# Performance work log

Measured on AMD Instinct MI355X. Metric: run time of the kernel, lower is better.

Reference implementation:

```python
import jax, jax.numpy as jnp
import numpy as np

N = 100000
E = 1600000
H = 128
M = 256
L = 6
G = 512          # number of graphs in the batch
A = 95           # num_atom_types
EXTRA = 3        # input_dim - 1
EPS = 1e-5


def swish(x):
    return x * jax.nn.sigmoid(x)


def setup_inputs() -> dict:
    key = jax.random.key(0)
    ks = jax.random.split(key, 16)
    z = jax.random.randint(ks[0], (N, 1), 0, A).astype(jnp.float32)
    extra = jax.random.normal(ks[1], (N, EXTRA), dtype=jnp.float32)
    x = jnp.concatenate([z, extra], axis=1)                     # [N, 4]
    edge_index = jax.random.randint(ks[2], (2, E), 0, N)        # [2, E]
    batch = jnp.sort(jax.random.randint(ks[3], (N,), 0, G))     # [N]
    s = 0.02
    z_embed = jax.random.normal(ks[4], (A, H), dtype=jnp.float32) * s
    extra_w = jax.random.normal(ks[5], (H, EXTRA), dtype=jnp.float32) * (1.0 / np.sqrt(EXTRA))
    extra_b = jnp.zeros((H,), jnp.float32)
    conv_w = jax.random.normal(ks[6], (L, H, H), dtype=jnp.float32) * (1.0 / np.sqrt(H))
    conv_b = jnp.zeros((L, H), jnp.float32)
    gamma = jnp.ones((L, H), jnp.float32)
    beta = jnp.zeros((L, H), jnp.float32)
    mean_scale = jnp.ones((L, H), jnp.float32)
    mlp_w1 = jax.random.normal(ks[7], (L, M, H), dtype=jnp.float32) * (1.0 / np.sqrt(H))
    mlp_b1 = jnp.zeros((L, M), jnp.float32)
    mlp_w2 = jax.random.normal(ks[8], (L, H, M), dtype=jnp.float32) * (1.0 / np.sqrt(M))
    mlp_b2 = jnp.zeros((L, H), jnp.float32)
    return dict(x=x, edge_index=edge_index, batch=batch, z_embed=z_embed,
                extra_w=extra_w, extra_b=extra_b, conv_w=conv_w, conv_b=conv_b,
                gamma=gamma, beta=beta, mean_scale=mean_scale,
                mlp_w1=mlp_w1, mlp_b1=mlp_b1, mlp_w2=mlp_w2, mlp_b2=mlp_b2)


def gnn_forward(x, edge_index, batch, z_embed, extra_w, extra_b, conv_w, conv_b,
                gamma, beta, mean_scale, mlp_w1, mlp_b1, mlp_w2, mlp_b2):
    z = x[:, 0].astype(jnp.int32)
    h = z_embed[z] + x[:, 1:] @ extra_w.T + extra_b                 # [N, H]

    # GCN: add self loops, symmetric normalization (computed once; graph is static)
    loop = jnp.arange(N)
    src = jnp.concatenate([edge_index[0], loop])
    dst = jnp.concatenate([edge_index[1], loop])
    deg = jax.ops.segment_sum(jnp.ones_like(dst, jnp.float32), dst, num_segments=N)
    dinv = jnp.where(deg > 0, jax.lax.rsqrt(jnp.maximum(deg, 1.0)), 0.0)
    norm = (dinv[src] * dinv[dst])[:, None]                         # [E+N, 1]

    cnt = jax.ops.segment_sum(jnp.ones((N,), jnp.float32), batch, num_segments=G)[:, None]
    cnt = jnp.maximum(cnt, 1.0)

    for i in range(L):
        h_res = h
        # GCNConv
        xw = h @ conv_w[i].T
        agg = jax.ops.segment_sum(xw[src] * norm, dst, num_segments=N) + conv_b[i]
        # GraphNorm: gamma * (x - alpha*mean) / sqrt(var + eps) + beta, per graph
        mean = jax.ops.segment_sum(agg, batch, num_segments=G) / cnt   # [G, H]
        sub = agg - mean_scale[i] * mean[batch]
        var = jax.ops.segment_sum(sub * sub, batch, num_segments=G) / cnt
        hn = gamma[i] * sub * jax.lax.rsqrt(var[batch] + EPS) + beta[i]
        ha = swish(hn)
        # residual MLP
        h = swish(swish(ha @ mlp_w1[i].T + mlp_b1[i]) @ mlp_w2[i].T + mlp_b2[i]) + h_res
    return h


def reference(x, edge_index, batch, z_embed, extra_w, extra_b, conv_w, conv_b,
              gamma, beta, mean_scale, mlp_w1, mlp_b1, mlp_w2, mlp_b2):
    return gnn_forward(x, edge_index, batch, z_embed, extra_w, extra_b, conv_w, conv_b,
                       gamma, beta, mean_scale, mlp_w1, mlp_b1, mlp_w2, mlp_b2)
```

## Files before the change

### kernel.cpp

```cpp
#include <hip/hip_runtime.h>

#define NN 100000
#define EE 1600000
#define HH 128
#define MM 256
#define LL 6
#define GG 512
#define SCAN_NB ((NN + 1023) / 1024)

typedef __attribute__((ext_vector_type(8))) short short8;
typedef __attribute__((ext_vector_type(4))) float floatx4;

__device__ __forceinline__ float swishf(float v) {
    return v / (1.0f + __expf(-v));
}

__device__ __forceinline__ unsigned short f2bf(float f) {
    unsigned u = __builtin_bit_cast(unsigned, f);
    unsigned r = u + 0x7FFFu + ((u >> 16) & 1u);
    return (unsigned short)(r >> 16);
}

__device__ __forceinline__ float bf2f(unsigned short u) {
    return __builtin_bit_cast(float, (unsigned)u << 16);
}

__device__ __forceinline__ float2 bf2f2(unsigned u) {
    float2 r;
    r.x = __builtin_bit_cast(float, u << 16);
    r.y = __builtin_bit_cast(float, u & 0xFFFF0000u);
    return r;
}

__device__ __forceinline__ unsigned cvt2bf(float a, float b) {
    unsigned r;
    asm("v_cvt_pk_bf16_f32 %0, %1, %2" : "=v"(r) : "v"(a), "v"(b));
    return r;
}

__device__ __forceinline__ void unpack8(uint4 v, float* a) {
    float2 p0 = bf2f2(v.x), p1 = bf2f2(v.y), p2 = bf2f2(v.z), p3 = bf2f2(v.w);
    a[0] = p0.x; a[1] = p0.y; a[2] = p1.x; a[3] = p1.y;
    a[4] = p2.x; a[5] = p2.y; a[6] = p3.x; a[7] = p3.y;
}

__device__ __forceinline__ uint4 pack8(const float* o) {
    uint4 pk;
    pk.x = cvt2bf(o[0], o[1]);
    pk.y = cvt2bf(o[2], o[3]);
    pk.z = cvt2bf(o[4], o[5]);
    pk.w = cvt2bf(o[6], o[7]);
    return pk;
}

__device__ __forceinline__ uint2 pack4(const float* o) {
    uint2 pk;
    pk.x = cvt2bf(o[0], o[1]);
    pk.y = cvt2bf(o[2], o[3]);
    return pk;
}

__global__ void k_embed(const float* __restrict__ x, const float* __restrict__ z_embed,
                        const float* __restrict__ ew, const float* __restrict__ eb,
                        unsigned short* __restrict__ hb) {
    int idx = blockIdx.x * blockDim.x + threadIdx.x;
    if (idx >= NN * 32) return;
    int n = idx >> 5;
    int c0 = (idx & 31) << 2;
    const float* xr = x + (size_t)n * 4;
    int z = (int)xr[0];
    float x1 = xr[1], x2 = xr[2], x3 = xr[3];
    const float* ze = z_embed + (size_t)z * HH + c0;
    float o[4];
#pragma unroll
    for (int j = 0; j < 4; ++j) {
        int c = c0 + j;
        o[j] = ze[j] + x1 * ew[c * 3 + 0] + x2 * ew[c * 3 + 1] + x3 * ew[c * 3 + 2] + eb[c];
    }
    *(uint2*)(hb + (size_t)n * HH + c0) = pack4(o);
}

__global__ void k_f2bf3(const float* __restrict__ s1, unsigned short* __restrict__ d1, int n1,
                        const float* __restrict__ s2, unsigned short* __restrict__ d2, int n2,
                        const float* __restrict__ s3, unsigned short* __restrict__ d3, int n3) {
    int i = blockIdx.x * blockDim.x + threadIdx.x;
    if (i < n1) {
        d1[i] = f2bf(s1[i]);
    } else if (i < n1 + n2) {
        d2[i - n1] = f2bf(s2[i - n1]);
    } else if (i < n1 + n2 + n3) {
        d3[i - n1 - n2] = f2bf(s3[i - n1 - n2]);
    }
}

__global__ __launch_bounds__(256) void k_degree_p(const int* __restrict__ dst,
                                                  int* __restrict__ deg) {
    int part = blockIdx.x & 7;
    int blk = blockIdx.x >> 3;
    int nb = gridDim.x >> 3;
    int lo = (int)((long long)part * NN / 8);
    int hi = (int)((long long)(part + 1) * NN / 8);
    for (int e = blk * 256 + threadIdx.x; e < EE; e += nb * 256) {
        int d = dst[e];
        if (d >= lo && d < hi) atomicAdd(&deg[d], 1);
    }
}

__global__ void k_dinv(const int* __restrict__ deg, float* __restrict__ dinv) {
    int n = blockIdx.x * blockDim.x + threadIdx.x;
    if (n < NN) dinv[n] = rsqrtf((float)(deg[n] + 1));
}

__global__ void k_scan1(const int* __restrict__ deg, int* __restrict__ bsum) {
    __shared__ int sd[256];
    int t = threadIdx.x;
    int base = blockIdx.x * 1024 + t * 4;
    int s = 0;
#pragma unroll
    for (int j = 0; j < 4; ++j) {
        int i = base + j;
        if (i < NN) s += deg[i];
    }
    sd[t] = s;
    __syncthreads();
    for (int off = 128; off > 0; off >>= 1) {
        if (t < off) sd[t] += sd[t + off];
        __syncthreads();
    }
    if (t == 0) bsum[blockIdx.x] = sd[0];
}

__global__ void k_scan2(const int* __restrict__ bsum, int* __restrict__ boff) {
    __shared__ int sd[128];
    int t = threadIdx.x;
    int v = (t < SCAN_NB) ? bsum[t] : 0;
    sd[t] = v;
    __syncthreads();
    for (int off = 1; off < 128; off <<= 1) {
        int u = (t >= off) ? sd[t - off] : 0;
        __syncthreads();
        sd[t] += u;
        __syncthreads();
    }
    boff[t] = sd[t] - v;
}

__global__ void k_scan3(const int* __restrict__ deg, const int* __restrict__ boff,
                        int* __restrict__ rowptr) {
    __shared__ int sd[256];
    int t = threadIdx.x;
    int base = blockIdx.x * 1024 + t * 4;
    int v[4];
    int s = 0;
#pragma unroll
    for (int j = 0; j < 4; ++j) {
        int i = base + j;
        v[j] = (i < NN) ? deg[i] : 0;
        s += v[j];
    }
    sd[t] = s;
    __syncthreads();
    for (int off = 1; off < 256; off <<= 1) {
        int u = (t >= off) ? sd[t - off] : 0;
        __syncthreads();
        sd[t] += u;
        __syncthreads();
    }
    int run = boff[blockIdx.x] + sd[t] - s;
#pragma unroll
    for (int j = 0; j < 4; ++j) {
        int i = base + j;
        if (i < NN) rowptr[i] = run;
        if (i == NN - 1) rowptr[NN] = run + v[j];
        run += v[j];
    }
}

__global__ __launch_bounds__(256) void k_fill_p(const int* __restrict__ ei,
                                                const int* __restrict__ rowptr,
                                                int* __restrict__ cursor,
                                                int* __restrict__ col) {
    int part = blockIdx.x & 7;
    int blk = blockIdx.x >> 3;
    int nb = gridDim.x >> 3;
    int lo = (int)((long long)part * NN / 8);
    int hi = (int)((long long)(part + 1) * NN / 8);
    for (int e = blk * 256 + threadIdx.x; e < EE; e += nb * 256) {
        int d = ei[EE + e];
        if (d >= lo && d < hi) {
            int p = atomicAdd(&cursor[d], 1);
            col[rowptr[d] + p] = ei[e];
        }
    }
}

__global__ void k_gptr(const int* __restrict__ batch, int* __restrict__ gptr) {
    int n = blockIdx.x * blockDim.x + threadIdx.x;
    if (n >= NN) return;
    int b = batch[n];
    int pb = (n == 0) ? -1 : batch[n - 1];
    for (int g = pb + 1; g <= b; ++g) gptr[g] = n;
    if (n == NN - 1) {
        for (int g = b + 1; g <= GG; ++g) gptr[g] = NN;
    }
}

__global__ __launch_bounds__(256) void k_conv(const unsigned short* __restrict__ A,
                                              const unsigned short* __restrict__ B,
                                              const float* __restrict__ dinv,
                                              unsigned short* __restrict__ Cb) {
    __shared__ unsigned short Bs[128][HH + 8];
    const int tid = threadIdx.x;
    const int wave = tid >> 6;
    const int lane = tid & 63;
    const int quad = lane >> 4;
    const int l16 = lane & 15;
    const int wr = (wave & 1) << 6;
    const int wc = (wave >> 1) << 6;
    const int rowBase = blockIdx.x * 128;

    for (int i = tid; i < 128 * (HH / 8); i += 256) {
        int r = i / (HH / 8);
        int kk = (i % (HH / 8)) * 8;
        int rho = (r & 64) | ((r & 3) << 4) | ((r >> 2) & 15);
        *(uint4*)(&Bs[rho][kk]) = *(const uint4*)(B + (size_t)r * HH + kk);
    }

    floatx4 acc[4][4];
    const floatx4 zed = {0.f, 0.f, 0.f, 0.f};
#pragma unroll
    for (int i = 0; i < 4; ++i)
#pragma unroll
        for (int j = 0; j < 4; ++j) acc[i][j] = zed;

    int ar[4];
#pragma unroll
    for (int i = 0; i < 4; ++i) {
        int r = rowBase + wr + (i << 4) + l16;
        ar[i] = r < NN ? r : NN - 1;
    }

    __syncthreads();

#pragma unroll
    for (int ks = 0; ks < HH / 32; ++ks) {
        int k = (ks << 5) + (quad << 3);
        short8 a[4], b[4];
#pragma unroll
        for (int i = 0; i < 4; ++i) a[i] = *(const short8*)(A + (size_t)ar[i] * HH + k);
#pragma unroll
        for (int j = 0; j < 4; ++j) b[j] = *(const short8*)(&Bs[wc + (j << 4) + l16][k]);
#pragma unroll
        for (int i = 0; i < 4; ++i)
#pragma unroll
            for (int j = 0; j < 4; ++j)
                acc[i][j] =
                    __builtin_amdgcn_mfma_f32_16x16x32_bf16(a[i], b[j], acc[i][j], 0, 0, 0);
    }

    const int c0 = wc + (l16 << 2);
#pragma unroll
    for (int i = 0; i < 4; ++i) {
        int rb = rowBase + wr + (i << 4) + (quad << 2);
#pragma unroll
        for (int reg = 0; reg < 4; ++reg) {
            int r = rb + reg;
            if (r < NN) {
                float dv = dinv[r];
                float o[4];
#pragma unroll
                for (int j = 0; j < 4; ++j) o[j] = acc[i][j][reg] * dv;
                *(uint2*)(Cb + (size_t)r * HH + c0) = pack4(o);
            }
        }
    }
}

__global__ __launch_bounds__(256) void k_agg(const unsigned short* __restrict__ y,
                                             const int* __restrict__ rowptr,
                                             const int* __restrict__ col,
                                             const float* __restrict__ dinv,
                                             const float* __restrict__ cb,
                                             const int* __restrict__ batch,
                                             unsigned short* __restrict__ agg,
                                             float* __restrict__ S1g,
                                             float* __restrict__ S2g) {
    __shared__ float s1s[4][128];
    __shared__ float s2s[4][128];
    __shared__ int sg[4];
    int w = threadIdx.x >> 6;
    int lane = threadIdx.x & 63;
    int d = blockIdx.x * 4 + w;
    bool valid = d < NN;
    int grp = lane >> 4;
    int l16 = lane & 15;
    const uint4* yv = (const uint4*)y;
    float acc[8];
#pragma unroll
    for (int j = 0; j < 8; ++j) acc[j] = 0.f;
    if (grp == 0 && valid) {
        uint4 v = yv[(size_t)d * 16 + l16];
        unpack8(v, acc);
    }
    int beg = 0, end = 0;
    if (valid) {
        beg = rowptr[d];
        end = rowptr[d + 1];
    }
    for (int e = beg + grp; e < end; e += 4) {
        int s = col[e];
        uint4 v = yv[(size_t)s * 16 + l16];
        float b0[8];
        unpack8(v, b0);
#pragma unroll
        for (int k = 0; k < 8; ++k) acc[k] += b0[k];
    }
#pragma unroll
    for (int j = 0; j < 8; ++j) {
        acc[j] += __shfl_xor(acc[j], 16, 64);
        acc[j] += __shfl_xor(acc[j], 32, 64);
    }
    if (grp == 0) {
        if (valid) {
            float dv = dinv[d];
            float4 c0 = *(const float4*)(cb + l16 * 8);
            float4 c1 = *(const float4*)(cb + l16 * 8 + 4);
            float o[8];
            o[0] = acc[0] * dv + c0.x; o[1] = acc[1] * dv + c0.y;
            o[2] = acc[2] * dv + c0.z; o[3] = acc[3] * dv + c0.w;
            o[4] = acc[4] * dv + c1.x; o[5] = acc[5] * dv + c1.y;
            o[6] = acc[6] * dv + c1.z; o[7] = acc[7] * dv + c1.w;
            uint4 pk = pack8(o);
            *(uint4*)(agg + (size_t)d * HH + l16 * 8) = pk;
            float2 q0 = bf2f2(pk.x), q1 = bf2f2(pk.y), q2 = bf2f2(pk.z), q3 = bf2f2(pk.w);
            float orv[8] = {q0.x, q0.y, q1.x, q1.y, q2.x, q2.y, q3.x, q3.y};
#pragma unroll
            for (int j = 0; j < 8; ++j) {
                s1s[w][l16 * 8 + j] = orv[j];
                s2s[w][l16 * 8 + j] = orv[j] * orv[j];
            }
        } else {
#pragma unroll
            for (int j = 0; j < 8; ++j) {
                s1s[w][l16 * 8 + j] = 0.f;
                s2s[w][l16 * 8 + j] = 0.f;
            }
        }
        if (l16 == 0) sg[w] = valid ? batch[d] : -1;
    }
    __syncthreads();
    if (threadIdx.x < 128) {
        int c = threadIdx.x;
        int g0 = sg[0], g1 = sg[1], g2 = sg[2], g3 = sg[3];
        if (g0 >= 0 && g0 == g1 && g0 == g2 && g0 == g3) {
            float a = (s1s[0][c] + s1s[1][c]) + (s1s[2][c] + s1s[3][c]);
            float b = (s2s[0][c] + s2s[1][c]) + (s2s[2][c] + s2s[3][c]);
            atomicAdd(&S1g[g0 * HH + c], a);
            atomicAdd(&S2g[g0 * HH + c], b);
        } else {
            int gs[4] = {g0, g1, g2, g3};
#pragma unroll
            for (int ww = 0; ww < 4; ++ww) {
                if (gs[ww] >= 0) {
                    atomicAdd(&S1g[gs[ww] * HH + c], s1s[ww][c]);
                    atomicAdd(&S2g[gs[ww] * HH + c], s2s[ww][c]);
                }
            }
        }
    }
}

__global__ __launch_bounds__(128) void k_finalize(const int* __restrict__ gptr,
                                                  const float* __restrict__ ms,
                                                  const float* __restrict__ gamma,
                                                  const float* __restrict__ beta,
                                                  float* __restrict__ S1g,
                                                  float* __restrict__ S2g,
                                                  float* __restrict__ c1,
                                                  float* __restrict__ c0) {
    int g = blockIdx.x;
    int c = threadIdx.x;
    int cnt = gptr[g + 1] - gptr[g];
    float inv = 1.0f / (float)(cnt > 0 ? cnt : 1);
    float S1 = S1g[g * HH + c];
    float S2 = S2g[g * HH + c];
    float m = S1 * inv;
    float msc = ms[c];
    float var = S2 * inv - msc * (2.0f - msc) * m * m;
    float rstd = rsqrtf(var + 1e-5f);
    float c1v = gamma[c] * rstd;
    c1[g * HH + c] = c1v;
    c0[g * HH + c] = beta[c] - c1v * msc * m;
    S1g[g * HH + c] = 0.f;
    S2g[g * HH + c] = 0.f;
}

__global__ __launch_bounds__(256, 4) void k_mega(const unsigned short* __restrict__ agg,
                                                 const int* __restrict__ batch,
                                                 const float* __restrict__ c1,
                                                 const float* __restrict__ c0,
                                                 const unsigned short* __restrict__ W1,
                                                 const float* __restrict__ b1,
                                                 const unsigned short* __restrict__ W2,
                                                 const float* __restrict__ b2,
                                                 const unsigned short* __restrict__ Wc,
                                                 const float* __restrict__ dinv,
                                                 unsigned short* __restrict__ hb,
                                                 float* __restrict__ h_out,
                                                 unsigned short* __restrict__ y_out,
                                                 int writeF, int doConv) {
    __shared__ unsigned short ha_s[64 * 136];
    __shared__ unsigned short ts[64 * 136];
    const int tid = threadIdx.x;
    const int wave = tid >> 6;
    const int lane = tid & 63;
    const int quad = lane >> 4;
    const int l16 = lane & 15;
    const int rowBase = blockIdx.x * 64;
    const floatx4 zed = {0.f, 0.f, 0.f, 0.f};

    {
        int lr = tid >> 2;
        int coff = (tid & 3) << 5;
        int r = rowBase + lr;
        if (r >= NN) r = NN - 1;
        int g = batch[r];
        const float* c1p = c1 + g * HH + coff;
        const float* c0p = c0 + g * HH + coff;
#pragma unroll
        for (int q = 0; q < 4; ++q) {
            uint4 raw = *(const uint4*)(agg + (size_t)r * HH + coff + (q << 3));
            float v[8];
            unpack8(raw, v);
            float4 ca = *(const float4*)(c1p + (q << 3));
            float4 cb4 = *(const float4*)(c1p + (q << 3) + 4);
            float4 da = *(const float4*)(c0p + (q << 3));
            float4 db = *(const float4*)(c0p + (q << 3) + 4);
            float cc1[8] = {ca.x, ca.y, ca.z, ca.w, cb4.x, cb4.y, cb4.z, cb4.w};
            float cc0[8] = {da.x, da.y, da.z, da.w, db.x, db.y, db.z, db.w};
            float o[8];
#pragma unroll
            for (int j = 0; j < 8; ++j) o[j] = swishf(cc1[j] * v[j] + cc0[j]);
            *(uint4*)(&ha_s[lr * 136 + coff + (q << 3)]) = pack8(o);
        }
    }
    __syncthreads();

    const int wrb = (wave & 1) << 5;
    const int wcb = (wave >> 1) << 6;
    const int co = wcb + (l16 << 2);
    {
        floatx4 acc2[2][4];
#pragma unroll
        for (int i = 0; i < 2; ++i)
#pragma unroll
            for (int j = 0; j < 4; ++j) acc2[i][j] = zed;

#pragma unroll
        for (int h = 0; h < 2; ++h) {
            floatx4 acc1[4][2];
#pragma unroll
            for (int i = 0; i < 4; ++i)
#pragma unroll
                for (int j = 0; j < 2; ++j) acc1[i][j] = zed;
            const int tcol = (wave << 5) + (l16 << 1);
#pragma unroll
            for (int ks = 0; ks < 4; ++ks) {
                int k = (ks << 5) + (quad << 3);
                short8 a[4], b[2];
#pragma unroll
                for (int i = 0; i < 4; ++i)
                    a[i] = *(const short8*)(&ha_s[((i << 4) + l16) * 136 + k]);
#pragma unroll
                for (int j = 0; j < 2; ++j)
                    b[j] = *(const short8*)(W1 + (size_t)((h << 7) + tcol + j) * HH + k);
#pragma unroll
                for (int i = 0; i < 4; ++i)
#pragma unroll
                    for (int j = 0; j < 2; ++j)
                        acc1[i][j] = __builtin_amdgcn_mfma_f32_16x16x32_bf16(a[i], b[j],
                                                                             acc1[i][j], 0, 0, 0);
            }
            float2 bv = *(const float2*)(b1 + (h << 7) + tcol);
#pragma unroll
            for (int i = 0; i < 4; ++i) {
#pragma unroll
                for (int reg = 0; reg < 4; ++reg) {
                    int lr = (i << 4) + (quad << 2) + reg;
                    float o0 = swishf(acc1[i][0][reg] + bv.x);
                    float o1 = swishf(acc1[i][1][reg] + bv.y);
                    *(unsigned*)(&ts[lr * 136 + tcol]) = cvt2bf(o0, o1);
                }
            }
            __syncthreads();

#pragma unroll
            for (int ks = 0; ks < 4; ++ks) {
                int k = (ks << 5) + (quad << 3);
                short8 a[2], b[4];
#pragma unroll
                for (int i = 0; i < 2; ++i)
                    a[i] = *(const short8*)(&ts[(wrb + (i << 4) + l16) * 136 + k]);
#pragma unroll
                for (int j = 0; j < 4; ++j)
                    b[j] = *(const short8*)(W2 + (size_t)(wcb + (l16 << 2) + j) * MM +
                                            (h << 7) + k);
#pragma unroll
                for (int i = 0; i < 2; ++i)
#pragma unroll
                    for (int j = 0; j < 4; ++j)
                        acc2[i][j] = __builtin_amdgcn_mfma_f32_16x16x32_bf16(a[i], b[j],
                                                                             acc2[i][j], 0, 0, 0);
            }
            if (h == 0) __syncthreads();
        }

        float4 b4 = *(const float4*)(b2 + co);
        float bv[4] = {b4.x, b4.y, b4.z, b4.w};
#pragma unroll
        for (int i = 0; i < 2; ++i) {
#pragma unroll
            for (int reg = 0; reg < 4; ++reg) {
                int lr = wrb + (i << 4) + (quad << 2) + reg;
                int r = rowBase + lr;
                if (r < NN) {
                    uint2 rv = *(const uint2*)(hb + (size_t)r * HH + co);
                    float2 r01 = bf2f2(rv.x), r23 = bf2f2(rv.y);
                    float o[4];
                    o[0] = swishf(acc2[i][0][reg] + bv[0]) + r01.x;
                    o[1] = swishf(acc2[i][1][reg] + bv[1]) + r01.y;
                    o[2] = swishf(acc2[i][2][reg] + bv[2]) + r23.x;
                    o[3] = swishf(acc2[i][3][reg] + bv[3]) + r23.y;
                    uint2 pk = pack4(o);
                    *(uint2*)(hb + (size_t)r * HH + co) = pk;
                    if (writeF)
                        *(float4*)(h_out + (size_t)r * HH + co) =
                            make_float4(o[0], o[1], o[2], o[3]);
                    *(uint2*)(&ha_s[lr * 136 + co]) = pk;
                } else {
                    *(uint2*)(&ha_s[lr * 136 + co]) = make_uint2(0u, 0u);
                }
            }
        }
    }

    if (doConv) {
        __syncthreads();
        floatx4 acc3[2][4];
#pragma unroll
        for (int i = 0; i < 2; ++i)
#pragma unroll
            for (int j = 0; j < 4; ++j) acc3[i][j] = zed;
#pragma unroll
        for (int ks = 0; ks < 4; ++ks) {
            int k = (ks << 5) + (quad << 3);
            short8 a[2], b[4];
#pragma unroll
            for (int i = 0; i < 2; ++i)
                a[i] = *(const short8*)(&ha_s[(wrb + (i << 4) + l16) * 136 + k]);
#pragma unroll
            for (int j = 0; j < 4; ++j)
                b[j] = *(const short8*)(Wc + (size_t)(wcb + (l16 << 2) + j) * HH + k);
#pragma unroll
            for (int i = 0; i < 2; ++i)
#pragma unroll
                for (int j = 0; j < 4; ++j)
                    acc3[i][j] =
                        __builtin_amdgcn_mfma_f32_16x16x32_bf16(a[i], b[j], acc3[i][j], 0, 0, 0);
        }
#pragma unroll
        for (int i = 0; i < 2; ++i) {
#pragma unroll
            for (int reg = 0; reg < 4; ++reg) {
                int r = rowBase + wrb + (i << 4) + (quad << 2) + reg;
                if (r < NN) {
                    float dv = dinv[r];
                    float o[4];
#pragma unroll
                    for (int j = 0; j < 4; ++j) o[j] = acc3[i][j][reg] * dv;
                    *(uint2*)(y_out + (size_t)r * HH + co) = pack4(o);
                }
            }
        }
    }
}

extern "C" void kernel_launch(void* const* d_in, const int* in_sizes, int n_in,
                              void* d_out, int out_size, void* d_ws, size_t ws_size,
                              hipStream_t stream) {
    const float* x = (const float*)d_in[0];
    const int* ei = (const int*)d_in[1];
    const int* batch = (const int*)d_in[2];
    const float* z_embed = (const float*)d_in[3];
    const float* extra_w = (const float*)d_in[4];
    const float* extra_b = (const float*)d_in[5];
    const float* conv_w = (const float*)d_in[6];
    const float* conv_b = (const float*)d_in[7];
    const float* gamma = (const float*)d_in[8];
    const float* beta = (const float*)d_in[9];
    const float* mean_scale = (const float*)d_in[10];
    const float* mlp_w1 = (const float*)d_in[11];
    const float* mlp_b1 = (const float*)d_in[12];
    const float* mlp_w2 = (const float*)d_in[13];
    const float* mlp_b2 = (const float*)d_in[14];
    float* h_out = (float*)d_out;

    char* wsB = (char*)d_ws;
    size_t off = 0;
    auto alloc = [&](size_t bytes) -> void* {
        void* p = (void*)(wsB + off);
        off = (off + bytes + 255) & ~(size_t)255;
        return p;
    };
    float* dinv = (float*)alloc((size_t)NN * 4);
    int* deg = (int*)alloc((size_t)NN * 4);
    int* cursor = (int*)alloc((size_t)NN * 4);
    int* rowptr = (int*)alloc((size_t)(NN + 1) * 4);
    int* bsum = (int*)alloc(128 * 4);
    int* boff = (int*)alloc(128 * 4);
    int* col = (int*)alloc((size_t)EE * 4);
    int* gptr = (int*)alloc((size_t)(GG + 1) * 4);
    float* c1t = (float*)alloc((size_t)GG * HH * 4);
    float* c0t = (float*)alloc((size_t)GG * HH * 4);
    float* S1g = (float*)alloc((size_t)GG * HH * 4);
    float* S2g = (float*)alloc((size_t)GG * HH * 4);
    unsigned short* wb =
        (unsigned short*)alloc((size_t)(LL * (HH * HH + MM * HH + HH * MM)) * 2);
    unsigned short* cwb = wb;
    unsigned short* w1b = wb + (size_t)LL * HH * HH;
    unsigned short* w2b = w1b + (size_t)LL * MM * HH;
    unsigned short* hb = (unsigned short*)alloc((size_t)NN * HH * 2);
    unsigned short* ybuf = (unsigned short*)alloc((size_t)NN * HH * 2);
    unsigned short* aggb = (unsigned short*)alloc((size_t)NN * HH * 2);

    hipMemsetAsync(deg, 0, (size_t)NN * 4, stream);
    hipMemsetAsync(cursor, 0, (size_t)NN * 4, stream);
    hipMemsetAsync(S1g, 0, (size_t)GG * HH * 4, stream);
    hipMemsetAsync(S2g, 0, (size_t)GG * HH * 4, stream);

    k_embed<<<(NN * 32 + 255) / 256, 256, 0, stream>>>(x, z_embed, extra_w, extra_b, hb);
    {
        int n1 = LL * HH * HH, n2 = LL * MM * HH, n3 = LL * HH * MM;
        int nt = n1 + n2 + n3;
        k_f2bf3<<<(nt + 255) / 256, 256, 0, stream>>>(conv_w, cwb, n1, mlp_w1, w1b, n2,
                                                      mlp_w2, w2b, n3);
    }
    k_degree_p<<<1024, 256, 0, stream>>>(ei + EE, deg);
    k_dinv<<<(NN + 255) / 256, 256, 0, stream>>>(deg, dinv);
    k_scan1<<<SCAN_NB, 256, 0, stream>>>(deg, bsum);
    k_scan2<<<1, 128, 0, stream>>>(bsum, boff);
    k_scan3<<<SCAN_NB, 256, 0, stream>>>(deg, boff, rowptr);
    k_fill_p<<<1024, 256, 0, stream>>>(ei, rowptr, cursor, col);
    k_gptr<<<(NN + 255) / 256, 256, 0, stream>>>(batch, gptr);

    int gconv = (NN + 127) / 128;
    int gmega = (NN + 63) / 64;
    k_conv<<<gconv, 256, 0, stream>>>(hb, cwb, dinv, ybuf);
    for (int i = 0; i < LL; ++i) {
        k_agg<<<(NN + 3) / 4, 256, 0, stream>>>(ybuf, rowptr, col, dinv,
                                                conv_b + (size_t)i * HH, batch, aggb, S1g,
                                                S2g);
        k_finalize<<<GG, 128, 0, stream>>>(gptr, mean_scale + (size_t)i * HH,
                                           gamma + (size_t)i * HH, beta + (size_t)i * HH,
                                           S1g, S2g, c1t, c0t);
        k_mega<<<gmega, 256, 0, stream>>>(
            aggb, batch, c1t, c0t, w1b + (size_t)i * MM * HH, mlp_b1 + (size_t)i * MM,
            w2b + (size_t)i * HH * MM, mlp_b2 + (size_t)i * HH,
            cwb + (size_t)(i + 1 < LL ? i + 1 : 0) * HH * HH, dinv, hb, h_out, ybuf,
            i == LL - 1 ? 1 : 0, i < LL - 1 ? 1 : 0);
    }
}
```

Measured before the change: 1.283 ms.

## Fold GraphNorm finalize into MLP kernel and batch four nodes per aggregation wave

Removes the per-layer finalize kernel. The MLP kernel now computes mean, variance and rstd directly from per-layer S1/S2 sums, and those sums sit in separate buffers for each of the six layers, so no reset is needed. Each aggregation wave now handles four consecutive nodes and accumulates per-graph statistics in registers, flushing atomics only when the graph changes; this reduces shared-memory and atomic traffic. The swish division is replaced with a fast reciprocal, and the last layer skips the bf16 h and shared-memory writes. The tradeoff is that the normalization coefficients are recomputed redundantly for every row in the MLP kernel, and the aggregation grid assumes N divides by 16.

```diff
diff --git a/kernel.cpp b/kernel.cpp
--- a/kernel.cpp
+++ b/kernel.cpp
@@ -12,7 +12,7 @@
 typedef __attribute__((ext_vector_type(4))) float floatx4;
 
 __device__ __forceinline__ float swishf(float v) {
-    return v / (1.0f + __expf(-v));
+    return v * __builtin_amdgcn_rcpf(1.0f + __expf(-v));
 }
 
 __device__ __forceinline__ unsigned short f2bf(float f) {
@@ -290,63 +290,89 @@
     __shared__ int sg[4];
     int w = threadIdx.x >> 6;
     int lane = threadIdx.x & 63;
-    int d = blockIdx.x * 4 + w;
-    bool valid = d < NN;
     int grp = lane >> 4;
     int l16 = lane & 15;
     const uint4* yv = (const uint4*)y;
-    float acc[8];
-#pragma unroll
-    for (int j = 0; j < 8; ++j) acc[j] = 0.f;
-    if (grp == 0 && valid) {
-        uint4 v = yv[(size_t)d * 16 + l16];
-        unpack8(v, acc);
-    }
-    int beg = 0, end = 0;
-    if (valid) {
-        beg = rowptr[d];
-        end = rowptr[d + 1];
-    }
-    for (int e = beg + grp; e < end; e += 4) {
-        int s = col[e];
-        uint4 v = yv[(size_t)s * 16 + l16];
-        float b0[8];
-        unpack8(v, b0);
-#pragma unroll
-        for (int k = 0; k < 8; ++k) acc[k] += b0[k];
-    }
-#pragma unroll
-    for (int j = 0; j < 8; ++j) {
-        acc[j] += __shfl_xor(acc[j], 16, 64);
-        acc[j] += __shfl_xor(acc[j], 32, 64);
-    }
-    if (grp == 0) {
-        if (valid) {
+    const int dbase = blockIdx.x * 16 + w * 4;
+
+    float cbv[8];
+    {
+        float4 c0 = *(const float4*)(cb + l16 * 8);
+        float4 c1 = *(const float4*)(cb + l16 * 8 + 4);
+        cbv[0] = c0.x; cbv[1] = c0.y; cbv[2] = c0.z; cbv[3] = c0.w;
+        cbv[4] = c1.x; cbv[5] = c1.y; cbv[6] = c1.z; cbv[7] = c1.w;
+    }
+
+    float sA[8], sB[8];
+#pragma unroll
+    for (int j = 0; j < 8; ++j) { sA[j] = 0.f; sB[j] = 0.f; }
+    int gcur = -1;
+
+    for (int i = 0; i < 4; ++i) {
+        int d = dbase + i;
+        float acc[8];
+#pragma unroll
+        for (int j = 0; j < 8; ++j) acc[j] = 0.f;
+        if (grp == 0) {
+            uint4 v = yv[(size_t)d * 16 + l16];
+            unpack8(v, acc);
+        }
+        int beg = rowptr[d];
+        int end = rowptr[d + 1];
+        for (int e = beg + grp; e < end; e += 4) {
+            int s = col[e];
+            uint4 v = yv[(size_t)s * 16 + l16];
+            float b0[8];
+            unpack8(v, b0);
+#pragma unroll
+            for (int k = 0; k < 8; ++k) acc[k] += b0[k];
+        }
+#pragma unroll
+        for (int j = 0; j < 8; ++j) {
+            acc[j] += __shfl_xor(acc[j], 16, 64);
+            acc[j] += __shfl_xor(acc[j], 32, 64);
+        }
+        if (grp == 0) {
             float dv = dinv[d];
-            float4 c0 = *(const float4*)(cb + l16 * 8);
-            float4 c1 = *(const float4*)(cb + l16 * 8 + 4);
             float o[8];
-            o[0] = acc[0] * dv + c0.x; o[1] = acc[1] * dv + c0.y;
-            o[2] = acc[2] * dv + c0.z; o[3] = acc[3] * dv + c0.w;
-            o[4] = acc[4] * dv + c1.x; o[5] = acc[5] * dv + c1.y;
-            o[6] = acc[6] * dv + c1.z; o[7] = acc[7] * dv + c1.w;
+#pragma unroll
+            for (int j = 0; j < 8; ++j) o[j] = acc[j] * dv + cbv[j];
             uint4 pk = pack8(o);
             *(uint4*)(agg + (size_t)d * HH + l16 * 8) = pk;
             float2 q0 = bf2f2(pk.x), q1 = bf2f2(pk.y), q2 = bf2f2(pk.z), q3 = bf2f2(pk.w);
             float orv[8] = {q0.x, q0.y, q1.x, q1.y, q2.x, q2.y, q3.x, q3.y};
-#pragma unroll
-            for (int j = 0; j < 8; ++j) {
-                s1s[w][l16 * 8 + j] = orv[j];
-                s2s[w][l16 * 8 + j] = orv[j] * orv[j];
-            }
-        } else {
-#pragma unroll
-            for (int j = 0; j < 8; ++j) {
-                s1s[w][l16 * 8 + j] = 0.f;
-                s2s[w][l16 * 8 + j] = 0.f;
-            }
-        }
-        if (l16 == 0) sg[w] = valid ? batch[d] : -1;
+            int g = batch[d];
+            if (g != gcur) {
+                if (gcur >= 0) {
+#pragma unroll
+                    for (int j = 0; j < 8; ++j) {
+                        atomicAdd(&S1g[gcur * HH + l16 * 8 + j], sA[j]);
+                        atomicAdd(&S2g[gcur * HH + l16 * 8 + j], sB[j]);
+                    }
+                }
+                gcur = g;
+#pragma unroll
+                for (int j = 0; j < 8; ++j) {
+                    sA[j] = orv[j];
+                    sB[j] = orv[j] * orv[j];
+                }
+            } else {
+#pragma unroll
+                for (int j = 0; j < 8; ++j) {
+                    sA[j] += orv[j];
+                    sB[j] += orv[j] * orv[j];
+                }
+            }
+        }
+    }
+
+    if (grp == 0) {
+#pragma unroll
+        for (int j = 0; j < 8; ++j) {
+            s1s[w][l16 * 8 + j] = sA[j];
+            s2s[w][l16 * 8 + j] = sB[j];
+        }
+        if (l16 == 0) sg[w] = gcur;
     }
     __syncthreads();
     if (threadIdx.x < 128) {
@@ -370,35 +396,14 @@
     }
 }
 
-__global__ __launch_bounds__(128) void k_finalize(const int* __restrict__ gptr,
-                                                  const float* __restrict__ ms,
-                                                  const float* __restrict__ gamma,
-                                                  const float* __restrict__ beta,
-                                                  float* __restrict__ S1g,
-                                                  float* __restrict__ S2g,
-                                                  float* __restrict__ c1,
-                                                  float* __restrict__ c0) {
-    int g = blockIdx.x;
-    int c = threadIdx.x;
-    int cnt = gptr[g + 1] - gptr[g];
-    float inv = 1.0f / (float)(cnt > 0 ? cnt : 1);
-    float S1 = S1g[g * HH + c];
-    float S2 = S2g[g * HH + c];
-    float m = S1 * inv;
-    float msc = ms[c];
-    float var = S2 * inv - msc * (2.0f - msc) * m * m;
-    float rstd = rsqrtf(var + 1e-5f);
-    float c1v = gamma[c] * rstd;
-    c1[g * HH + c] = c1v;
-    c0[g * HH + c] = beta[c] - c1v * msc * m;
-    S1g[g * HH + c] = 0.f;
-    S2g[g * HH + c] = 0.f;
-}
-
 __global__ __launch_bounds__(256, 4) void k_mega(const unsigned short* __restrict__ agg,
                                                  const int* __restrict__ batch,
-                                                 const float* __restrict__ c1,
-                                                 const float* __restrict__ c0,
+                                                 const int* __restrict__ gptr,
+                                                 const float* __restrict__ ms,
+                                                 const float* __restrict__ gamma,
+                                                 const float* __restrict__ beta,
+                                                 const float* __restrict__ S1,
+                                                 const float* __restrict__ S2,
                                                  const unsigned short* __restrict__ W1,
                                                  const float* __restrict__ b1,
                                                  const unsigned short* __restrict__ W2,
@@ -425,22 +430,30 @@
         int r = rowBase + lr;
         if (r >= NN) r = NN - 1;
         int g = batch[r];
-        const float* c1p = c1 + g * HH + coff;
-        const float* c0p = c0 + g * HH + coff;
+        int cnt = gptr[g + 1] - gptr[g];
+        float inv = 1.0f / (float)(cnt > 0 ? cnt : 1);
+        const float* S1p = S1 + g * HH + coff;
+        const float* S2p = S2 + g * HH + coff;
+        const float* msp = ms + coff;
+        const float* gap = gamma + coff;
+        const float* bep = beta + coff;
 #pragma unroll
         for (int q = 0; q < 4; ++q) {
             uint4 raw = *(const uint4*)(agg + (size_t)r * HH + coff + (q << 3));
             float v[8];
             unpack8(raw, v);
-            float4 ca = *(const float4*)(c1p + (q << 3));
-            float4 cb4 = *(const float4*)(c1p + (q << 3) + 4);
-            float4 da = *(const float4*)(c0p + (q << 3));
-            float4 db = *(const float4*)(c0p + (q << 3) + 4);
-            float cc1[8] = {ca.x, ca.y, ca.z, ca.w, cb4.x, cb4.y, cb4.z, cb4.w};
-            float cc0[8] = {da.x, da.y, da.z, da.w, db.x, db.y, db.z, db.w};
             float o[8];
 #pragma unroll
-            for (int j = 0; j < 8; ++j) o[j] = swishf(cc1[j] * v[j] + cc0[j]);
+            for (int j = 0; j < 8; ++j) {
+                int c = (q << 3) + j;
+                float m = S1p[c] * inv;
+                float msc = msp[c];
+                float var = S2p[c] * inv - msc * (2.0f - msc) * m * m;
+                float rstd = rsqrtf(var + 1e-5f);
+                float c1v = gap[c] * rstd;
+                float c0v = bep[c] - c1v * msc * m;
+                o[j] = swishf(c1v * v[j] + c0v);
+            }
             *(uint4*)(&ha_s[lr * 136 + coff + (q << 3)]) = pack8(o);
         }
     }
@@ -531,13 +544,15 @@
                     o[1] = swishf(acc2[i][1][reg] + bv[1]) + r01.y;
                     o[2] = swishf(acc2[i][2][reg] + bv[2]) + r23.x;
                     o[3] = swishf(acc2[i][3][reg] + bv[3]) + r23.y;
-                    uint2 pk = pack4(o);
-                    *(uint2*)(hb + (size_t)r * HH + co) = pk;
-                    if (writeF)
+                    if (doConv) {
+                        uint2 pk = pack4(o);
+                        *(uint2*)(hb + (size_t)r * HH + co) = pk;
+                        *(uint2*)(&ha_s[lr * 136 + co]) = pk;
+                    } else {
                         *(float4*)(h_out + (size_t)r * HH + co) =
                             make_float4(o[0], o[1], o[2], o[3]);
-                    *(uint2*)(&ha_s[lr * 136 + co]) = pk;
-                } else {
+                    }
+                } else if (doConv) {
                     *(uint2*)(&ha_s[lr * 136 + co]) = make_uint2(0u, 0u);
                 }
             }
@@ -620,10 +635,8 @@
     int* boff = (int*)alloc(128 * 4);
     int* col = (int*)alloc((size_t)EE * 4);
     int* gptr = (int*)alloc((size_t)(GG + 1) * 4);
-    float* c1t = (float*)alloc((size_t)GG * HH * 4);
-    float* c0t = (float*)alloc((size_t)GG * HH * 4);
-    float* S1g = (float*)alloc((size_t)GG * HH * 4);
-    float* S2g = (float*)alloc((size_t)GG * HH * 4);
+    float* S1g6 = (float*)alloc((size_t)LL * GG * HH * 4);
+    float* S2g6 = (float*)alloc((size_t)LL * GG * HH * 4);
     unsigned short* wb =
         (unsigned short*)alloc((size_t)(LL * (HH * HH + MM * HH + HH * MM)) * 2);
     unsigned short* cwb = wb;
@@ -635,8 +648,8 @@
 
     hipMemsetAsync(deg, 0, (size_t)NN * 4, stream);
     hipMemsetAsync(cursor, 0, (size_t)NN * 4, stream);
-    hipMemsetAsync(S1g, 0, (size_t)GG * HH * 4, stream);
-    hipMemsetAsync(S2g, 0, (size_t)GG * HH * 4, stream);
+    hipMemsetAsync(S1g6, 0, (size_t)LL * GG * HH * 4, stream);
+    hipMemsetAsync(S2g6, 0, (size_t)LL * GG * HH * 4, stream);
 
     k_embed<<<(NN * 32 + 255) / 256, 256, 0, stream>>>(x, z_embed, extra_w, extra_b, hb);
     {
@@ -657,15 +670,14 @@
     int gmega = (NN + 63) / 64;
     k_conv<<<gconv, 256, 0, stream>>>(hb, cwb, dinv, ybuf);
     for (int i = 0; i < LL; ++i) {
-        k_agg<<<(NN + 3) / 4, 256, 0, stream>>>(ybuf, rowptr, col, dinv,
-                                                conv_b + (size_t)i * HH, batch, aggb, S1g,
-                                                S2g);
-        k_finalize<<<GG, 128, 0, stream>>>(gptr, mean_scale + (size_t)i * HH,
-                                           gamma + (size_t)i * HH, beta + (size_t)i * HH,
-                                           S1g, S2g, c1t, c0t);
+        float* S1 = S1g6 + (size_t)i * GG * HH;
+        float* S2 = S2g6 + (size_t)i * GG * HH;
+        k_agg<<<NN / 16, 256, 0, stream>>>(ybuf, rowptr, col, dinv,
+                                           conv_b + (size_t)i * HH, batch, aggb, S1, S2);
         k_mega<<<gmega, 256, 0, stream>>>(
-            aggb, batch, c1t, c0t, w1b + (size_t)i * MM * HH, mlp_b1 + (size_t)i * MM,
-            w2b + (size_t)i * HH * MM, mlp_b2 + (size_t)i * HH,
+            aggb, batch, gptr, mean_scale + (size_t)i * HH, gamma + (size_t)i * HH,
+            beta + (size_t)i * HH, S1, S2, w1b + (size_t)i * MM * HH,
+            mlp_b1 + (size_t)i * MM, w2b + (size_t)i * HH * MM, mlp_b2 + (size_t)i * HH,
             cwb + (size_t)(i + 1 < LL ? i + 1 : 0) * HH * HH, dinv, hb, h_out, ybuf,
             i == LL - 1 ? 1 : 0, i < LL - 1 ? 1 : 0);
     }
```

Measured after the change: 1.343 ms. 1.05x slower.
